# Optimization experiments

Hardware: AMD Instinct MI355X
Metric: run time of the kernel (lower is better)

Reference implementation:

```python
import jax, jax.numpy as jnp
import numpy as np
import math

N_EMBD = 1024
NUM_HEADS = 16
HEAD_DIM = N_EMBD // NUM_HEADS


def alibi_slopes(num_heads):
    x = (2 ** 8) ** (1.0 / num_heads)
    return jnp.array([1.0 / x ** (i + 1) for i in range(num_heads)], dtype=jnp.float32)


def setup_inputs() -> dict:
    key = jax.random.key(0)
    k1, k2 = jax.random.split(key)
    x = jax.random.normal(k1, (2, 2048, N_EMBD), dtype=jnp.float32)
    W_kqv = jax.random.normal(k2, (3 * N_EMBD, N_EMBD), dtype=jnp.float32) * (1.0 / math.sqrt(N_EMBD))
    return {"x": x, "W_kqv": W_kqv}


def reference(x, W_kqv):
    B, S, E = x.shape
    H, D = NUM_HEADS, HEAD_DIM
    kqv = jnp.einsum('bse,fe->bsf', x, W_kqv)  # Linear without bias
    k, q, v = jnp.split(kqv, 3, axis=-1)       # chunk order: key, query, value
    # [B, H, S, D]
    q = q.reshape(B, S, H, D).transpose(0, 2, 1, 3)
    k = k.reshape(B, S, H, D).transpose(0, 2, 1, 3)
    v = v.reshape(B, S, H, D).transpose(0, 2, 1, 3)
    # ALiBi bias: slopes[h] * (j - i), shape [H, S, S]
    rel = jnp.arange(S)[None, :] - jnp.arange(S)[:, None]  # [S, S]
    bias = alibi_slopes(H)[:, None, None] * rel.astype(jnp.float32)
    scale = math.sqrt(E)  # NOTE: module scales by sqrt(n_embd), not sqrt(head_dim)
    score = jnp.einsum('bhqd,bhkd->bhqk', q, k) / scale + bias[None]
    causal = jnp.tril(jnp.ones((S, S), dtype=bool))
    score = jnp.where(causal[None, None], score, -jnp.inf)
    attn = jax.nn.softmax(score, axis=-1)
    out = jnp.einsum('bhqk,bhkd->bhqd', attn, v)
    return out.transpose(0, 2, 1, 3).reshape(B, S, E)
```

## Files before the change

kernel.cpp:

```cpp
#include <hip/hip_runtime.h>
#include <hip/hip_bf16.h>
#include <math.h>

#define TOTAL_B 2
#define SEQ 2048
#define EMB 1024
#define NH 16
#define HD 64
#define M_GEMM (TOTAL_B*SEQ)
#define N_GEMM (3*EMB)
#define K_GEMM EMB

typedef __attribute__((ext_vector_type(8))) short short8;
typedef __attribute__((ext_vector_type(4))) float f32x4;
typedef __attribute__((ext_vector_type(4))) unsigned u32x4;

static __device__ __forceinline__ short f2bf(float f) {
  union { float f; unsigned u; } v; v.f = f;
  unsigned r = v.u + 0x7fff + ((v.u >> 16) & 1u);
  return (short)(r >> 16);
}

static __device__ __forceinline__ void gload_lds16(const void* g, void* l) {
  __builtin_amdgcn_global_load_lds(
      (const __attribute__((address_space(1))) void*)(uintptr_t)g,
      (__attribute__((address_space(3))) void*)(uintptr_t)l, 16, 0, 0);
}

static __device__ __forceinline__ float exp2v(float x) {
  float r; asm("v_exp_f32 %0, %1" : "=v"(r) : "v"(x)); return r;
}
static __device__ __forceinline__ unsigned cvtpk(float lo, float hi) {
  unsigned r; asm("v_cvt_pk_bf16_f32 %0, %1, %2" : "=v"(r) : "v"(lo), "v"(hi)); return r;
}
static __device__ __forceinline__ void pl32swap(unsigned &a, unsigned &b) {
  asm("v_permlane32_swap_b32 %0, %1" : "+v"(a), "+v"(b));
}

__global__ void cvt_kernel(const float* __restrict__ x, const float* __restrict__ w,
                           short* __restrict__ xb, short* __restrict__ wb) {
  const long nx = (long)M_GEMM * K_GEMM;
  const long nw = (long)N_GEMM * K_GEMM;
  long i = (long)blockIdx.x * blockDim.x + threadIdx.x;
  const long tot = (nx + nw) / 8;
  if (i >= tot) return;
  long e = i * 8;
  const float* s; short* d;
  if (e < nx) { s = x + e; d = xb + e; }
  else        { s = w + (e - nx); d = wb + (e - nx); }
  float4 a = ((const float4*)s)[0];
  float4 b = ((const float4*)s)[1];
  short8 o;
  o[0]=f2bf(a.x); o[1]=f2bf(a.y); o[2]=f2bf(a.z); o[3]=f2bf(a.w);
  o[4]=f2bf(b.x); o[5]=f2bf(b.y); o[6]=f2bf(b.z); o[7]=f2bf(b.w);
  *(short8*)d = o;
}

__global__ __launch_bounds__(256) void qkv_gemm(const short* __restrict__ A, const short* __restrict__ Bm,
                                                short* __restrict__ Kb, short* __restrict__ Qb,
                                                short* __restrict__ Vb) {
  __shared__ __align__(16) short As[128*64];
  __shared__ __align__(16) short Bs[128*64];
  const int tid = threadIdx.x;
  const int lane = tid & 63, wid = tid >> 6;
  const int lr = lane & 15, lg = lane >> 4;
  const int m0 = blockIdx.y * 128, n0 = blockIdx.x * 128;
  const int wm = (wid >> 1) * 64, wn = (wid & 1) * 64;

  f32x4 acc[4][4] = {};

  for (int kt = 0; kt < K_GEMM/64; ++kt) {
#pragma unroll
    for (int i = 0; i < 4; ++i) {
      const int e16 = i*256 + tid;
      const int row = e16 >> 3;
      const int ch  = e16 & 7;
      const int sch = ch ^ (row & 7);
      const short* ga = A  + (size_t)(m0 + row)*K_GEMM + kt*64 + sch*8;
      gload_lds16(ga, As + i*2048 + wid*512);
      const short* gb = Bm + (size_t)(n0 + row)*K_GEMM + kt*64 + sch*8;
      gload_lds16(gb, Bs + i*2048 + wid*512);
    }
    __syncthreads();
#pragma unroll
    for (int kk = 0; kk < 2; ++kk) {
      short8 af[4], bfr[4];
#pragma unroll
      for (int mi = 0; mi < 4; ++mi) {
        const int r = wm + mi*16 + lr;
        const int c = (kk*4 + lg) ^ (r & 7);
        af[mi] = *(const short8*)(As + r*64 + c*8);
      }
#pragma unroll
      for (int ni = 0; ni < 4; ++ni) {
        const int r = wn + ni*16 + lr;
        const int c = (kk*4 + lg) ^ (r & 7);
        bfr[ni] = *(const short8*)(Bs + r*64 + c*8);
      }
#pragma unroll
      for (int mi = 0; mi < 4; ++mi)
#pragma unroll
        for (int ni = 0; ni < 4; ++ni)
          acc[mi][ni] = __builtin_amdgcn_mfma_f32_16x16x32_bf16(af[mi], bfr[ni], acc[mi][ni], 0, 0, 0);
    }
    __syncthreads();
  }

#pragma unroll
  for (int mi = 0; mi < 4; ++mi) {
#pragma unroll
    for (int ni = 0; ni < 4; ++ni) {
#pragma unroll
      for (int r = 0; r < 4; ++r) {
        const int m = m0 + wm + mi*16 + lg*4 + r;
        const int f = n0 + wn + ni*16 + lr;
        const int b = m >> 11, s = m & 2047;
        const int which = f >> 10, fl = f & 1023;
        const int h = fl >> 6, d = fl & 63;
        short* dst = (which == 0) ? Kb : (which == 1) ? Qb : Vb;
        float val = acc[mi][ni][r];
        if (which == 1) val *= 0.04508422f;
        dst[((size_t)((b*NH + h)*SEQ + s))*HD + d] = f2bf(val);
      }
    }
  }
}

__global__ void vtrans(const short* __restrict__ Vb, short* __restrict__ Vt) {
  __shared__ short t[64][72];
  const int hb = blockIdx.y;
  const int s0 = blockIdx.x * 64;
  const short* src = Vb + ((size_t)hb*SEQ + s0)*HD;
  short* dst = Vt + (size_t)hb*HD*SEQ;
  const int tid = threadIdx.x;
#pragma unroll
  for (int i = 0; i < 2; ++i) {
    const int e = i*2048 + tid*8;
    const int r = e >> 6, c = e & 63;
    short8 v = *(const short8*)(src + (size_t)r*HD + c);
#pragma unroll
    for (int j = 0; j < 8; ++j) t[r][c+j] = v[j];
  }
  __syncthreads();
#pragma unroll
  for (int i = 0; i < 2; ++i) {
    const int e = i*2048 + tid*8;
    const int d = e >> 6, ss = e & 63;
    short8 v;
#pragma unroll
    for (int j = 0; j < 8; ++j) v[j] = t[ss+j][d];
    *(short8*)(dst + (size_t)d*SEQ + s0 + ss) = v;
  }
}

__global__ __launch_bounds__(256, 4) void attn_kernel(const short* __restrict__ Kb, const short* __restrict__ Qb,
                                                      const short* __restrict__ Vt, float* __restrict__ Out) {
  __shared__ __align__(16) short Ks[2][64*64];
  __shared__ __align__(16) short Vs[2][64*64];
  const int tid = threadIdx.x, lane = tid & 63, wid = tid >> 6;
  const int lr = lane & 15, lg = lane >> 4;
  const int bh = blockIdx.x;
  const int b = bh >> 4, h = bh & 15;
  const int qidx = blockIdx.y;
  const int g = qidx >> 3, rq = qidx & 7;
  const int qt = (g == 0) ? rq : (g == 1) ? (15 - rq) : (g == 2) ? (16 + rq) : (31 - rq);
  const float slope = exp2f(-0.5f * (float)(h + 1)) * 1.44269504f;
  const short* Kp = Kb + (size_t)bh * SEQ * HD;
  const short* Qp = Qb + (size_t)bh * SEQ * HD;
  const short* Vp = Vt + (size_t)bh * HD * SEQ;
  float* Ob = Out + (size_t)b * SEQ * EMB + (size_t)h * HD;

  const int q0 = qt * 64, qrb = q0 + wid * 16;
  const int nt = qt + 1;

  short8 qf[2];
#pragma unroll
  for (int kk = 0; kk < 2; ++kk)
    qf[kk] = *(const short8*)(Qp + (size_t)(qrb + lr)*HD + kk*32 + lg*8);

  const int bp = ((lr & 4) << 1) | ((lr & 2) << 1) | ((lr & 8) >> 2) | (lr & 1);
  const int cbase = qrb + lr - ((lg & 1) * 8 + (lg >> 1) * 2);

  float m_run = -INFINITY, l_run = 0.f;
  f32x4 o[4] = {};

  auto stage = [&](int buf, int t) {
    const int kv0 = t * 64;
#pragma unroll
    for (int i = 0; i < 2; ++i) {
      const int e16 = i*256 + tid;
      const int row = e16 >> 3, ch = e16 & 7;
      const int sch = ch ^ (row & 7);
      gload_lds16(Kp + (size_t)(kv0 + row)*HD + sch*8, &Ks[buf][i*2048 + wid*512]);
      gload_lds16(Vp + (size_t)row*SEQ + kv0 + sch*8,  &Vs[buf][i*2048 + wid*512]);
    }
  };

  int cur = 0;
  stage(0, 0);
  __syncthreads();

#pragma unroll 1
  for (int t = 0; t < nt; ++t) {
    const int kv0 = t * 64;
    if (t + 1 < nt) stage(cur ^ 1, t + 1);

    if (kv0 <= qrb + 15) {
      short8 kf[4][2];
#pragma unroll
      for (int kvf = 0; kvf < 4; ++kvf) {
        const int row = kvf*16 + bp;
#pragma unroll
        for (int kk = 0; kk < 2; ++kk) {
          const int c = (kk*4 + lg) ^ (row & 7);
          kf[kvf][kk] = *(const short8*)(&Ks[cur][row*64 + c*8]);
        }
      }
      f32x4 sc[4];
      __builtin_amdgcn_s_setprio(1);
#pragma unroll
      for (int kvf = 0; kvf < 4; ++kvf) {
        f32x4 s = {};
        s = __builtin_amdgcn_mfma_f32_16x16x32_bf16(kf[kvf][0], qf[0], s, 0, 0, 0);
        s = __builtin_amdgcn_mfma_f32_16x16x32_bf16(kf[kvf][1], qf[1], s, 0, 0, 0);
        sc[kvf] = s;
      }
      __builtin_amdgcn_s_setprio(0);

      const float dbase = (float)(kv0 - cbase);
      const bool needMask = (kv0 + 63 > qrb);
      float v[4][4];
#pragma unroll
      for (int kvf = 0; kvf < 4; ++kvf) {
#pragma unroll
        for (int r = 0; r < 4; ++r) {
          const float C = (float)(kvf*16 + (r>>1)*4 + (r&1));
          const float toff = dbase + C;
          float val = fmaf(slope, toff, sc[kvf][r]);
          if (needMask && toff > 0.f) val = -INFINITY;
          v[kvf][r] = val;
        }
      }
      float q0m = fmaxf(fmaxf(v[0][0], v[0][1]), fmaxf(v[0][2], v[0][3]));
      float q1m = fmaxf(fmaxf(v[1][0], v[1][1]), fmaxf(v[1][2], v[1][3]));
      float q2m = fmaxf(fmaxf(v[2][0], v[2][1]), fmaxf(v[2][2], v[2][3]));
      float q3m = fmaxf(fmaxf(v[3][0], v[3][1]), fmaxf(v[3][2], v[3][3]));
      float mt = fmaxf(fmaxf(q0m, q1m), fmaxf(q2m, q3m));
      mt = fmaxf(mt, __shfl_xor(mt, 16, 64));
      mt = fmaxf(mt, __shfl_xor(mt, 32, 64));

      if (__any(mt > m_run + 10.f)) {
        const float mn = fmaxf(m_run, mt);
        const float corr = exp2v(m_run - mn);
        m_run = mn;
        l_run *= corr;
        float co[4];
#pragma unroll
        for (int r = 0; r < 4; ++r) co[r] = __shfl(corr, lg*4 + r, 64);
#pragma unroll
        for (int dt = 0; dt < 4; ++dt)
#pragma unroll
          for (int r = 0; r < 4; ++r) o[dt][r] *= co[r];
      }
#pragma unroll
      for (int kvf = 0; kvf < 4; ++kvf)
#pragma unroll
        for (int r = 0; r < 4; ++r)
          v[kvf][r] = exp2v(v[kvf][r] - m_run);
      float s0 = (v[0][0]+v[0][1]) + (v[0][2]+v[0][3]);
      float s1 = (v[1][0]+v[1][1]) + (v[1][2]+v[1][3]);
      float s2 = (v[2][0]+v[2][1]) + (v[2][2]+v[2][3]);
      float s3 = (v[3][0]+v[3][1]) + (v[3][2]+v[3][3]);
      float lt = (s0+s1) + (s2+s3);
      lt += __shfl_xor(lt, 16, 64);
      lt += __shfl_xor(lt, 32, 64);
      l_run += lt;

      unsigned pk[4][2];
#pragma unroll
      for (int kvf = 0; kvf < 4; ++kvf) {
        pk[kvf][0] = cvtpk(v[kvf][0], v[kvf][1]);
        pk[kvf][1] = cvtpk(v[kvf][2], v[kvf][3]);
      }
      __builtin_amdgcn_s_setprio(1);
#pragma unroll
      for (int ks = 0; ks < 2; ++ks) {
        unsigned w0 = pk[2*ks][0], w1 = pk[2*ks+1][0];
        pl32swap(w0, w1);
        unsigned w2 = pk[2*ks][1], w3 = pk[2*ks+1][1];
        pl32swap(w2, w3);
        u32x4 wv = {w0, w1, w2, w3};
        const short8 pf = __builtin_bit_cast(short8, wv);
#pragma unroll
        for (int dt = 0; dt < 4; ++dt) {
          const int rv = dt*16 + lr;
          const int cv = (ks*4 + lg) ^ (rv & 7);
          const short8 vf = *(const short8*)(&Vs[cur][rv*64 + cv*8]);
          o[dt] = __builtin_amdgcn_mfma_f32_16x16x32_bf16(pf, vf, o[dt], 0, 0, 0);
        }
      }
      __builtin_amdgcn_s_setprio(0);
    }
    __syncthreads();
    cur ^= 1;
  }

  const float inv = 1.f / l_run;
  float li[4];
#pragma unroll
  for (int r = 0; r < 4; ++r) li[r] = __shfl(inv, lg*4 + r, 64);
#pragma unroll
  for (int dt = 0; dt < 4; ++dt)
#pragma unroll
    for (int r = 0; r < 4; ++r) {
      const int iq = qrb + lg*4 + r;
      Ob[(size_t)iq*EMB + dt*16 + lr] = o[dt][r] * li[r];
    }
}

extern "C" void kernel_launch(void* const* d_in, const int* in_sizes, int n_in,
                              void* d_out, int out_size, void* d_ws, size_t ws_size,
                              hipStream_t stream) {
  const float* x = (const float*)d_in[0];
  const float* w = (const float*)d_in[1];
  char* ws = (char*)d_ws;
  if (ws_size < 39845888u) return;
  short* xb = (short*)(ws);
  short* wb = (short*)(ws + 8388608u);
  short* Kb = (short*)(ws + 14680064u);
  short* Qb = (short*)(ws + 23068672u);
  short* Vb = (short*)(ws + 31457280u);
  short* Vt = xb;
  float* out = (float*)d_out;

  cvt_kernel<<<3584, 256, 0, stream>>>(x, w, xb, wb);
  qkv_gemm<<<dim3(N_GEMM/128, M_GEMM/128), 256, 0, stream>>>(xb, wb, Kb, Qb, Vb);
  vtrans<<<dim3(SEQ/64, TOTAL_B*NH), 256, 0, stream>>>(Vb, Vt);
  attn_kernel<<<dim3(TOTAL_B*NH, 32), 256, 0, stream>>>(Kb, Qb, Vt, out);
}
```

Baseline: 107.5 us.

## Software-pipeline QK^T one tile ahead with triple-buffered K staging

Splits K and V staging, triple-buffers K so it is loaded two tiles ahead, and computes the next tile's QK^T scores before the current tile's softmax and PV. The goal is to overlap MFMA work with the exp/max softmax work and with global-to-LDS loads. It also changes the query-tile ordering to a simple reverse order, longest blocks first, and only applies the causal mask on the diagonal tile. The cost is more LDS and more live registers (two score sets), which may reduce occupancy under the launch bounds.

```diff
diff --git a/kernel.cpp b/kernel.cpp
--- a/kernel.cpp
+++ b/kernel.cpp
@@ -155,15 +155,13 @@
 
 __global__ __launch_bounds__(256, 4) void attn_kernel(const short* __restrict__ Kb, const short* __restrict__ Qb,
                                                       const short* __restrict__ Vt, float* __restrict__ Out) {
-  __shared__ __align__(16) short Ks[2][64*64];
+  __shared__ __align__(16) short Ks[3][64*64];
   __shared__ __align__(16) short Vs[2][64*64];
   const int tid = threadIdx.x, lane = tid & 63, wid = tid >> 6;
   const int lr = lane & 15, lg = lane >> 4;
   const int bh = blockIdx.x;
   const int b = bh >> 4, h = bh & 15;
-  const int qidx = blockIdx.y;
-  const int g = qidx >> 3, rq = qidx & 7;
-  const int qt = (g == 0) ? rq : (g == 1) ? (15 - rq) : (g == 2) ? (16 + rq) : (31 - rq);
+  const int qt = 31 - blockIdx.y;
   const float slope = exp2f(-0.5f * (float)(h + 1)) * 1.44269504f;
   const short* Kp = Kb + (size_t)bh * SEQ * HD;
   const short* Qp = Qb + (size_t)bh * SEQ * HD;
@@ -184,7 +182,7 @@
   float m_run = -INFINITY, l_run = 0.f;
   f32x4 o[4] = {};
 
-  auto stage = [&](int buf, int t) {
+  auto stageK = [&](int buf, int t) {
     const int kv0 = t * 64;
 #pragma unroll
     for (int i = 0; i < 2; ++i) {
@@ -192,117 +190,141 @@
       const int row = e16 >> 3, ch = e16 & 7;
       const int sch = ch ^ (row & 7);
       gload_lds16(Kp + (size_t)(kv0 + row)*HD + sch*8, &Ks[buf][i*2048 + wid*512]);
-      gload_lds16(Vp + (size_t)row*SEQ + kv0 + sch*8,  &Vs[buf][i*2048 + wid*512]);
     }
   };
-
-  int cur = 0;
-  stage(0, 0);
+  auto stageV = [&](int buf, int t) {
+    const int kv0 = t * 64;
+#pragma unroll
+    for (int i = 0; i < 2; ++i) {
+      const int e16 = i*256 + tid;
+      const int row = e16 >> 3, ch = e16 & 7;
+      const int sch = ch ^ (row & 7);
+      gload_lds16(Vp + (size_t)row*SEQ + kv0 + sch*8, &Vs[buf][i*2048 + wid*512]);
+    }
+  };
+  auto qkt = [&](int buf, f32x4* sc) {
+    short8 kf[4][2];
+#pragma unroll
+    for (int kvf = 0; kvf < 4; ++kvf) {
+      const int row = kvf*16 + bp;
+#pragma unroll
+      for (int kk = 0; kk < 2; ++kk) {
+        const int c = (kk*4 + lg) ^ (row & 7);
+        kf[kvf][kk] = *(const short8*)(&Ks[buf][row*64 + c*8]);
+      }
+    }
+    __builtin_amdgcn_s_setprio(1);
+#pragma unroll
+    for (int kvf = 0; kvf < 4; ++kvf) {
+      f32x4 s = {};
+      s = __builtin_amdgcn_mfma_f32_16x16x32_bf16(kf[kvf][0], qf[0], s, 0, 0, 0);
+      s = __builtin_amdgcn_mfma_f32_16x16x32_bf16(kf[kvf][1], qf[1], s, 0, 0, 0);
+      sc[kvf] = s;
+    }
+    __builtin_amdgcn_s_setprio(0);
+  };
+
+  stageK(0, 0);
+  if (nt > 1) stageK(1, 1);
+  stageV(0, 0);
   __syncthreads();
-
+  f32x4 sc_cur[4], sc_next[4];
+  qkt(0, sc_cur);
+
+  int k1 = 1, k2 = 2;
 #pragma unroll 1
   for (int t = 0; t < nt; ++t) {
     const int kv0 = t * 64;
-    if (t + 1 < nt) stage(cur ^ 1, t + 1);
-
-    if (kv0 <= qrb + 15) {
-      short8 kf[4][2];
-#pragma unroll
-      for (int kvf = 0; kvf < 4; ++kvf) {
-        const int row = kvf*16 + bp;
-#pragma unroll
-        for (int kk = 0; kk < 2; ++kk) {
-          const int c = (kk*4 + lg) ^ (row & 7);
-          kf[kvf][kk] = *(const short8*)(&Ks[cur][row*64 + c*8]);
-        }
-      }
-      f32x4 sc[4];
-      __builtin_amdgcn_s_setprio(1);
-#pragma unroll
-      for (int kvf = 0; kvf < 4; ++kvf) {
-        f32x4 s = {};
-        s = __builtin_amdgcn_mfma_f32_16x16x32_bf16(kf[kvf][0], qf[0], s, 0, 0, 0);
-        s = __builtin_amdgcn_mfma_f32_16x16x32_bf16(kf[kvf][1], qf[1], s, 0, 0, 0);
-        sc[kvf] = s;
-      }
-      __builtin_amdgcn_s_setprio(0);
-
-      const float dbase = (float)(kv0 - cbase);
-      const bool needMask = (kv0 + 63 > qrb);
-      float v[4][4];
-#pragma unroll
-      for (int kvf = 0; kvf < 4; ++kvf) {
+    if (t + 2 < nt) stageK(k2, t + 2);
+    if (t + 1 < nt) stageV((t + 1) & 1, t + 1);
+    if (t + 1 < nt) qkt(k1, sc_next);
+
+    const float dbase = (float)(kv0 - cbase);
+    float v[4][4];
+    if (t == nt - 1) {
+#pragma unroll
+      for (int kvf = 0; kvf < 4; ++kvf)
 #pragma unroll
         for (int r = 0; r < 4; ++r) {
           const float C = (float)(kvf*16 + (r>>1)*4 + (r&1));
           const float toff = dbase + C;
-          float val = fmaf(slope, toff, sc[kvf][r]);
-          if (needMask && toff > 0.f) val = -INFINITY;
+          float val = fmaf(slope, toff, sc_cur[kvf][r]);
+          if (toff > 0.f) val = -INFINITY;
           v[kvf][r] = val;
         }
-      }
-      float q0m = fmaxf(fmaxf(v[0][0], v[0][1]), fmaxf(v[0][2], v[0][3]));
-      float q1m = fmaxf(fmaxf(v[1][0], v[1][1]), fmaxf(v[1][2], v[1][3]));
-      float q2m = fmaxf(fmaxf(v[2][0], v[2][1]), fmaxf(v[2][2], v[2][3]));
-      float q3m = fmaxf(fmaxf(v[3][0], v[3][1]), fmaxf(v[3][2], v[3][3]));
-      float mt = fmaxf(fmaxf(q0m, q1m), fmaxf(q2m, q3m));
-      mt = fmaxf(mt, __shfl_xor(mt, 16, 64));
-      mt = fmaxf(mt, __shfl_xor(mt, 32, 64));
-
-      if (__any(mt > m_run + 10.f)) {
-        const float mn = fmaxf(m_run, mt);
-        const float corr = exp2v(m_run - mn);
-        m_run = mn;
-        l_run *= corr;
-        float co[4];
-#pragma unroll
-        for (int r = 0; r < 4; ++r) co[r] = __shfl(corr, lg*4 + r, 64);
-#pragma unroll
-        for (int dt = 0; dt < 4; ++dt)
-#pragma unroll
-          for (int r = 0; r < 4; ++r) o[dt][r] *= co[r];
-      }
+    } else {
 #pragma unroll
       for (int kvf = 0; kvf < 4; ++kvf)
 #pragma unroll
-        for (int r = 0; r < 4; ++r)
-          v[kvf][r] = exp2v(v[kvf][r] - m_run);
-      float s0 = (v[0][0]+v[0][1]) + (v[0][2]+v[0][3]);
-      float s1 = (v[1][0]+v[1][1]) + (v[1][2]+v[1][3]);
-      float s2 = (v[2][0]+v[2][1]) + (v[2][2]+v[2][3]);
-      float s3 = (v[3][0]+v[3][1]) + (v[3][2]+v[3][3]);
-      float lt = (s0+s1) + (s2+s3);
-      lt += __shfl_xor(lt, 16, 64);
-      lt += __shfl_xor(lt, 32, 64);
-      l_run += lt;
-
-      unsigned pk[4][2];
-#pragma unroll
-      for (int kvf = 0; kvf < 4; ++kvf) {
-        pk[kvf][0] = cvtpk(v[kvf][0], v[kvf][1]);
-        pk[kvf][1] = cvtpk(v[kvf][2], v[kvf][3]);
-      }
-      __builtin_amdgcn_s_setprio(1);
-#pragma unroll
-      for (int ks = 0; ks < 2; ++ks) {
-        unsigned w0 = pk[2*ks][0], w1 = pk[2*ks+1][0];
-        pl32swap(w0, w1);
-        unsigned w2 = pk[2*ks][1], w3 = pk[2*ks+1][1];
-        pl32swap(w2, w3);
-        u32x4 wv = {w0, w1, w2, w3};
-        const short8 pf = __builtin_bit_cast(short8, wv);
-#pragma unroll
-        for (int dt = 0; dt < 4; ++dt) {
-          const int rv = dt*16 + lr;
-          const int cv = (ks*4 + lg) ^ (rv & 7);
-          const short8 vf = *(const short8*)(&Vs[cur][rv*64 + cv*8]);
-          o[dt] = __builtin_amdgcn_mfma_f32_16x16x32_bf16(pf, vf, o[dt], 0, 0, 0);
+        for (int r = 0; r < 4; ++r) {
+          const float C = (float)(kvf*16 + (r>>1)*4 + (r&1));
+          v[kvf][r] = fmaf(slope, dbase + C, sc_cur[kvf][r]);
         }
-      }
-      __builtin_amdgcn_s_setprio(0);
-    }
+    }
+    float q0m = fmaxf(fmaxf(v[0][0], v[0][1]), fmaxf(v[0][2], v[0][3]));
+    float q1m = fmaxf(fmaxf(v[1][0], v[1][1]), fmaxf(v[1][2], v[1][3]));
+    float q2m = fmaxf(fmaxf(v[2][0], v[2][1]), fmaxf(v[2][2], v[2][3]));
+    float q3m = fmaxf(fmaxf(v[3][0], v[3][1]), fmaxf(v[3][2], v[3][3]));
+    float mt = fmaxf(fmaxf(q0m, q1m), fmaxf(q2m, q3m));
+    mt = fmaxf(mt, __shfl_xor(mt, 16, 64));
+    mt = fmaxf(mt, __shfl_xor(mt, 32, 64));
+
+    if (__any(mt > m_run + 10.f)) {
+      const float mn = fmaxf(m_run, mt);
+      const float corr = exp2v(m_run - mn);
+      m_run = mn;
+      l_run *= corr;
+      float co[4];
+#pragma unroll
+      for (int r = 0; r < 4; ++r) co[r] = __shfl(corr, lg*4 + r, 64);
+#pragma unroll
+      for (int dt = 0; dt < 4; ++dt)
+#pragma unroll
+        for (int r = 0; r < 4; ++r) o[dt][r] *= co[r];
+    }
+#pragma unroll
+    for (int kvf = 0; kvf < 4; ++kvf)
+#pragma unroll
+      for (int r = 0; r < 4; ++r)
+        v[kvf][r] = exp2v(v[kvf][r] - m_run);
+    float s0 = (v[0][0]+v[0][1]) + (v[0][2]+v[0][3]);
+    float s1 = (v[1][0]+v[1][1]) + (v[1][2]+v[1][3]);
+    float s2 = (v[2][0]+v[2][1]) + (v[2][2]+v[2][3]);
+    float s3 = (v[3][0]+v[3][1]) + (v[3][2]+v[3][3]);
+    float lt = (s0+s1) + (s2+s3);
+    lt += __shfl_xor(lt, 16, 64);
+    lt += __shfl_xor(lt, 32, 64);
+    l_run += lt;
+
+    unsigned pk[4][2];
+#pragma unroll
+    for (int kvf = 0; kvf < 4; ++kvf) {
+      pk[kvf][0] = cvtpk(v[kvf][0], v[kvf][1]);
+      pk[kvf][1] = cvtpk(v[kvf][2], v[kvf][3]);
+    }
+    __builtin_amdgcn_s_setprio(1);
+#pragma unroll
+    for (int ks = 0; ks < 2; ++ks) {
+      unsigned w0 = pk[2*ks][0], w1 = pk[2*ks+1][0];
+      pl32swap(w0, w1);
+      unsigned w2 = pk[2*ks][1], w3 = pk[2*ks+1][1];
+      pl32swap(w2, w3);
+      u32x4 wv = {w0, w1, w2, w3};
+      const short8 pf = __builtin_bit_cast(short8, wv);
+#pragma unroll
+      for (int dt = 0; dt < 4; ++dt) {
+        const int rv = dt*16 + lr;
+        const int cv = (ks*4 + lg) ^ (rv & 7);
+        const short8 vf = *(const short8*)(&Vs[t & 1][rv*64 + cv*8]);
+        o[dt] = __builtin_amdgcn_mfma_f32_16x16x32_bf16(pf, vf, o[dt], 0, 0, 0);
+      }
+    }
+    __builtin_amdgcn_s_setprio(0);
+
     __syncthreads();
-    cur ^= 1;
+#pragma unroll
+    for (int kvf = 0; kvf < 4; ++kvf) sc_cur[kvf] = sc_next[kvf];
+    k1 = k2; k2 = (k2 == 2) ? 0 : k2 + 1;
   }
 
   const float inv = 1.f / l_run;
```

Result: faster. 100.4 us (-6.6%).
